# Performance work log

Hardware: AMD Instinct MI355X
Metric: run time of the kernel (lower is better)

## Reference

```python
import jax, jax.numpy as jnp
import numpy as np

ALPHA = 0.34          # Ewald splitting parameter (init kwarg alpha)
MAX_HKL = 12          # init kwarg max_hkl
TWO_PI = 2.0 * np.pi


def setup_inputs() -> dict:
    key = jax.random.key(0)
    k1, k2 = jax.random.split(key)
    N = 4096
    L = 40.0  # cubic box edge (Angstrom)
    coords = jax.random.uniform(k1, (N, 3), dtype=jnp.float32) * L
    q = jax.random.normal(k2, (N,), dtype=jnp.float32)
    q = q - jnp.mean(q)  # neutral cell (k=0 term is excluded)
    box = jnp.eye(3, dtype=jnp.float32) * L
    return {"coords": coords, "box": box, "q": q}


def _ewald_recip_energy(coords, box, q):
    """Reciprocal-space Ewald sum over |h|,|k|,|l| <= MAX_HKL (rank=0 PME fallback).

    pot_i = (4*pi/V) * sum_{k!=0} exp(-|k|^2/(4 a^2))/|k|^2 * Re[S(k) exp(-i k.r_i)]
    E     = 0.5 * sum_i q_i * pot_i
    """
    K = MAX_HKL
    vol = jnp.abs(jnp.linalg.det(box))
    recip = TWO_PI * jnp.linalg.inv(box).T  # rows = reciprocal lattice vectors (3,3)
    h = jnp.arange(-K, K + 1)
    hh, kk, ll = jnp.meshgrid(h, h, h, indexing="ij")
    hkl = jnp.stack([hh.ravel(), kk.ravel(), ll.ravel()], axis=-1).astype(jnp.float32)  # (Nk,3)
    kvecs = hkl @ recip                      # (Nk,3)
    k2 = jnp.sum(kvecs * kvecs, axis=-1)     # (Nk,)
    nonzero = k2 > 0.0                       # mask out k = 0 (static shape, jit-safe)
    k2_safe = jnp.where(nonzero, k2, 1.0)
    inv_4a2 = 1.0 / (4.0 * ALPHA * ALPHA)
    fac = jnp.where(nonzero, jnp.exp(-k2_safe * inv_4a2) / k2_safe, 0.0)  # (Nk,)
    phases = coords @ kvecs.T                # (N, Nk)
    c = jnp.cos(phases)
    s = jnp.sin(phases)
    Sre = q @ c                              # (Nk,) Re S(k)
    Sim = q @ s                              # (Nk,) Im S(k)
    pref = (4.0 * np.pi) / vol
    # Re[S(k) e^{-i k.r_i}] = Sre*cos + Sim*sin
    pot = pref * (c @ (fac * Sre) + s @ (fac * Sim))  # (N,)
    return 0.5 * jnp.sum(q * pot)


def reference(coords, box, q):
    return _ewald_recip_energy(coords, box, q)
```

## Files before the change

### kernel.cpp

```cpp
#include <hip/hip_runtime.h>
#include <math.h>

namespace {
constexpr int   KMAX   = 12;
constexpr int   NLINE  = 313;
constexpr int   NGROUP = NLINE * 5;
constexpr int   NKV    = NGROUP * 5;
constexpr int   NSLICE = 8;
constexpr int   SLICE_CAP = 512;
constexpr int   S2_BLOCKS = (NKV + 255) / 256;
constexpr float ALPHA_  = 0.34f;
constexpr float TWO_PI_ = 6.283185307179586f;
}

__device__ __forceinline__ void cofactors(const float* __restrict__ box,
                                          float C[3][3], float* det) {
  const float b00 = box[0], b01 = box[1], b02 = box[2];
  const float b10 = box[3], b11 = box[4], b12 = box[5];
  const float b20 = box[6], b21 = box[7], b22 = box[8];
  C[0][0] =  (b11 * b22 - b12 * b21);
  C[0][1] = -(b10 * b22 - b12 * b20);
  C[0][2] =  (b10 * b21 - b11 * b20);
  C[1][0] = -(b01 * b22 - b02 * b21);
  C[1][1] =  (b00 * b22 - b02 * b20);
  C[1][2] = -(b00 * b21 - b01 * b20);
  C[2][0] =  (b01 * b12 - b02 * b11);
  C[2][1] = -(b00 * b12 - b02 * b10);
  C[2][2] =  (b00 * b11 - b01 * b10);
  *det = b00 * C[0][0] + b01 * C[0][1] + b02 * C[0][2];
}

__device__ __forceinline__ void line_hk(int L, int* h, int* k) {
  if (L < 300)      { *h = L / 25 + 1; *k = L % 25 - 12; }
  else if (L < 312) { *h = 0;          *k = L - 299;     }
  else              { *h = 0;          *k = 0;           }
}

__global__ __launch_bounds__(256) void ewald_groups(
    const float* __restrict__ coords, const float* __restrict__ box,
    const float* __restrict__ q, int N, float* __restrict__ partial,
    float* __restrict__ out)
{
  __shared__ float4 sf[SLICE_CAP];

  if (blockIdx.x == 0 && blockIdx.y == 0 && threadIdx.x == 0) out[0] = 0.0f;

  float C[3][3], det;
  cofactors(box, C, &det);
  const float invdet = 1.0f / det;

  const int slice = blockIdx.y;
  const int sp    = (N + NSLICE - 1) / NSLICE;
  const int s_beg = slice * sp;
  const int s_end = min(s_beg + sp, N);

  const int lane = threadIdx.x & 63;
  const int g    = blockIdx.x * 4 + (threadIdx.x >> 6);
  const int gc   = (g < NGROUP) ? g : (NGROUP - 1);

  int h, k; line_hk(gc / 5, &h, &k);
  const float hf  = (float)h;
  const float kf  = (float)k;
  const float l0f = (float)(-KMAX + 5 * (gc % 5));

  float Sre[5] = {0.f, 0.f, 0.f, 0.f, 0.f};
  float Sim[5] = {0.f, 0.f, 0.f, 0.f, 0.f};

  for (int cb = s_beg; cb < s_end; cb += SLICE_CAP) {
    const int cnt = min(SLICE_CAP, s_end - cb);
    __syncthreads();
    for (int t = threadIdx.x; t < SLICE_CAP; t += 256) {
      float4 v = make_float4(0.f, 0.f, 0.f, 0.f);
      if (t < cnt) {
        const int gi = cb + t;
        const float x = coords[3 * gi + 0];
        const float y = coords[3 * gi + 1];
        const float z = coords[3 * gi + 2];
        v.x = (x * C[0][0] + y * C[0][1] + z * C[0][2]) * invdet;
        v.y = (x * C[1][0] + y * C[1][1] + z * C[1][2]) * invdet;
        float c = (x * C[2][0] + y * C[2][1] + z * C[2][2]) * invdet;
        v.z = c - floorf(c);
        v.w = q[gi];
      }
      sf[t] = v;
    }
    __syncthreads();

    for (int i = lane; i < SLICE_CAP; i += 64) {
      const float4 p = sf[i];
      float t = fmaf(hf, p.x, fmaf(kf, p.y, l0f * p.z));
      float tf;
      asm("v_fract_f32 %0, %1" : "=v"(tf) : "v"(t));
      float s0, c0, sr, cr;
      asm("v_sin_f32 %0, %1" : "=v"(s0) : "v"(tf));
      asm("v_cos_f32 %0, %1" : "=v"(c0) : "v"(tf));
      asm("v_sin_f32 %0, %1" : "=v"(sr) : "v"(p.z));
      asm("v_cos_f32 %0, %1" : "=v"(cr) : "v"(p.z));
      float Pre = p.w * c0, Pim = p.w * s0;
      Sre[0] += Pre; Sim[0] += Pim;
#pragma unroll
      for (int u = 1; u < 5; ++u) {
        const float nre = fmaf(Pre, cr, -(Pim * sr));
        const float nim = fmaf(Pre, sr,  (Pim * cr));
        Pre = nre; Pim = nim;
        Sre[u] += Pre; Sim[u] += Pim;
      }
    }
  }

#pragma unroll
  for (int off = 32; off > 0; off >>= 1) {
#pragma unroll
    for (int u = 0; u < 5; ++u) {
      Sre[u] += __shfl_down(Sre[u], off);
      Sim[u] += __shfl_down(Sim[u], off);
    }
  }
  if (g < NGROUP && lane == 0) {
    float* dst = partial + (size_t)(g * NSLICE + slice) * 10;
#pragma unroll
    for (int u = 0; u < 5; ++u) {
      dst[2 * u + 0] = Sre[u];
      dst[2 * u + 1] = Sim[u];
    }
  }
}

__global__ __launch_bounds__(256) void stage2(
    const float* __restrict__ partial, const float* __restrict__ box,
    float* __restrict__ out)
{
  __shared__ float red[256];
  const int idx = blockIdx.x * 256 + threadIdx.x;
  float e = 0.f;
  if (idx < NKV) {
    const int g = idx / 5, u = idx % 5;
    const int L = g / 5, sub = g % 5;
    int h, k; line_hk(L, &h, &k);
    const int l = -KMAX + 5 * sub + u;
    if (!(h == 0 && k == 0 && l <= 0)) {
      float re = 0.f, im = 0.f;
      for (int s = 0; s < NSLICE; ++s) {
        const float* p = partial + (size_t)(g * NSLICE + s) * 10 + 2 * u;
        re += p[0]; im += p[1];
      }
      float C[3][3], det;
      cofactors(box, C, &det);
      const float invdet = 1.0f / det;
      const float hf = (float)h, kf = (float)k, lf = (float)l;
      const float kx = (hf * C[0][0] + kf * C[1][0] + lf * C[2][0]) * invdet;
      const float ky = (hf * C[0][1] + kf * C[1][1] + lf * C[2][1]) * invdet;
      const float kz = (hf * C[0][2] + kf * C[1][2] + lf * C[2][2]) * invdet;
      const float k2 = TWO_PI_ * TWO_PI_ * (kx * kx + ky * ky + kz * kz);
      const float fac = __expf(-k2 / (4.0f * ALPHA_ * ALPHA_)) / k2;
      e = fac * fmaf(re, re, im * im);
    }
  }
  red[threadIdx.x] = e;
  __syncthreads();
  for (int s = 128; s > 0; s >>= 1) {
    if (threadIdx.x < s) red[threadIdx.x] += red[threadIdx.x + s];
    __syncthreads();
  }
  if (threadIdx.x == 0) {
    float C[3][3], det;
    cofactors(box, C, &det);
    const float scale = (4.0f * 3.14159265358979323846f) / fabsf(det);
    atomicAdd(out, scale * red[0]);
  }
}

extern "C" void kernel_launch(void* const* d_in, const int* in_sizes, int n_in,
                              void* d_out, int out_size, void* d_ws, size_t ws_size,
                              hipStream_t stream) {
  const float* coords = (const float*)d_in[0];
  const float* box    = (const float*)d_in[1];
  const float* q      = (const float*)d_in[2];
  float* out = (float*)d_out;
  const int N = in_sizes[2];

  float* partial = (float*)d_ws;

  const dim3 grid((NGROUP + 3) / 4, NSLICE);
  hipLaunchKernelGGL(ewald_groups, grid, dim3(256), 0, stream,
                     coords, box, q, N, partial, out);
  hipLaunchKernelGGL(stage2, dim3(S2_BLOCKS), dim3(256), 0, stream,
                     partial, box, out);
}
```

Before: 20.08 us.

## Precompute fractional coordinates in a separate kernel and drop LDS staging

Moves the per-atom conversion to fractional coordinates into a small prepass kernel that writes float4 records to workspace. The main structure-factor kernel then reads them straight from global memory (L2-cached) instead of staging through shared memory with two barriers per chunk, and gets launch bounds that allow higher occupancy. This removes redundant per-block coordinate transforms and syncs, at the cost of an extra kernel launch and a global round trip.

```diff
diff --git a/kernel.cpp b/kernel.cpp
--- a/kernel.cpp
+++ b/kernel.cpp
@@ -7,7 +7,6 @@
 constexpr int   NGROUP = NLINE * 5;
 constexpr int   NKV    = NGROUP * 5;
 constexpr int   NSLICE = 8;
-constexpr int   SLICE_CAP = 512;
 constexpr int   S2_BLOCKS = (NKV + 255) / 256;
 constexpr float ALPHA_  = 0.34f;
 constexpr float TWO_PI_ = 6.283185307179586f;
@@ -36,24 +35,32 @@
   else              { *h = 0;          *k = 0;           }
 }
 
-__global__ __launch_bounds__(256) void ewald_groups(
+__global__ __launch_bounds__(256) void make_frac(
     const float* __restrict__ coords, const float* __restrict__ box,
-    const float* __restrict__ q, int N, float* __restrict__ partial,
+    const float* __restrict__ q, int N, float4* __restrict__ frac,
     float* __restrict__ out)
 {
-  __shared__ float4 sf[SLICE_CAP];
-
-  if (blockIdx.x == 0 && blockIdx.y == 0 && threadIdx.x == 0) out[0] = 0.0f;
-
+  const int i = blockIdx.x * 256 + threadIdx.x;
+  if (i == 0) out[0] = 0.0f;
+  if (i >= N) return;
   float C[3][3], det;
   cofactors(box, C, &det);
   const float invdet = 1.0f / det;
+  const float x = coords[3 * i + 0];
+  const float y = coords[3 * i + 1];
+  const float z = coords[3 * i + 2];
+  float4 f;
+  f.x = (x * C[0][0] + y * C[0][1] + z * C[0][2]) * invdet;
+  f.y = (x * C[1][0] + y * C[1][1] + z * C[1][2]) * invdet;
+  float c = (x * C[2][0] + y * C[2][1] + z * C[2][2]) * invdet;
+  f.z = c - floorf(c);
+  f.w = q[i];
+  frac[i] = f;
+}
 
-  const int slice = blockIdx.y;
-  const int sp    = (N + NSLICE - 1) / NSLICE;
-  const int s_beg = slice * sp;
-  const int s_end = min(s_beg + sp, N);
-
+__global__ __launch_bounds__(256, 8) void ewald_g5(
+    const float4* __restrict__ frac, int N, float* __restrict__ partial)
+{
   const int lane = threadIdx.x & 63;
   const int g    = blockIdx.x * 4 + (threadIdx.x >> 6);
   const int gc   = (g < NGROUP) ? g : (NGROUP - 1);
@@ -63,48 +70,32 @@
   const float kf  = (float)k;
   const float l0f = (float)(-KMAX + 5 * (gc % 5));
 
+  const int slice = blockIdx.y;
+  const int sp    = (N + NSLICE - 1) / NSLICE;
+  const int s_beg = slice * sp;
+  const int s_end = min(s_beg + sp, N);
+
   float Sre[5] = {0.f, 0.f, 0.f, 0.f, 0.f};
   float Sim[5] = {0.f, 0.f, 0.f, 0.f, 0.f};
 
-  for (int cb = s_beg; cb < s_end; cb += SLICE_CAP) {
-    const int cnt = min(SLICE_CAP, s_end - cb);
-    __syncthreads();
-    for (int t = threadIdx.x; t < SLICE_CAP; t += 256) {
-      float4 v = make_float4(0.f, 0.f, 0.f, 0.f);
-      if (t < cnt) {
-        const int gi = cb + t;
-        const float x = coords[3 * gi + 0];
-        const float y = coords[3 * gi + 1];
-        const float z = coords[3 * gi + 2];
-        v.x = (x * C[0][0] + y * C[0][1] + z * C[0][2]) * invdet;
-        v.y = (x * C[1][0] + y * C[1][1] + z * C[1][2]) * invdet;
-        float c = (x * C[2][0] + y * C[2][1] + z * C[2][2]) * invdet;
-        v.z = c - floorf(c);
-        v.w = q[gi];
-      }
-      sf[t] = v;
-    }
-    __syncthreads();
-
-    for (int i = lane; i < SLICE_CAP; i += 64) {
-      const float4 p = sf[i];
-      float t = fmaf(hf, p.x, fmaf(kf, p.y, l0f * p.z));
-      float tf;
-      asm("v_fract_f32 %0, %1" : "=v"(tf) : "v"(t));
-      float s0, c0, sr, cr;
-      asm("v_sin_f32 %0, %1" : "=v"(s0) : "v"(tf));
-      asm("v_cos_f32 %0, %1" : "=v"(c0) : "v"(tf));
-      asm("v_sin_f32 %0, %1" : "=v"(sr) : "v"(p.z));
-      asm("v_cos_f32 %0, %1" : "=v"(cr) : "v"(p.z));
-      float Pre = p.w * c0, Pim = p.w * s0;
-      Sre[0] += Pre; Sim[0] += Pim;
+  for (int i = s_beg + lane; i < s_end; i += 64) {
+    const float4 p = frac[i];
+    float t = fmaf(hf, p.x, fmaf(kf, p.y, l0f * p.z));
+    float tf;
+    asm("v_fract_f32 %0, %1" : "=v"(tf) : "v"(t));
+    float s0, c0, sr, cr;
+    asm("v_sin_f32 %0, %1" : "=v"(s0) : "v"(tf));
+    asm("v_cos_f32 %0, %1" : "=v"(c0) : "v"(tf));
+    asm("v_sin_f32 %0, %1" : "=v"(sr) : "v"(p.z));
+    asm("v_cos_f32 %0, %1" : "=v"(cr) : "v"(p.z));
+    float Pre = p.w * c0, Pim = p.w * s0;
+    Sre[0] += Pre; Sim[0] += Pim;
 #pragma unroll
-      for (int u = 1; u < 5; ++u) {
-        const float nre = fmaf(Pre, cr, -(Pim * sr));
-        const float nim = fmaf(Pre, sr,  (Pim * cr));
-        Pre = nre; Pim = nim;
-        Sre[u] += Pre; Sim[u] += Pim;
-      }
+    for (int u = 1; u < 5; ++u) {
+      const float nre = fmaf(Pre, cr, -(Pim * sr));
+      const float nim = fmaf(Pre, sr,  (Pim * cr));
+      Pre = nre; Pim = nim;
+      Sre[u] += Pre; Sim[u] += Pim;
     }
   }
 
@@ -179,11 +170,13 @@
   float* out = (float*)d_out;
   const int N = in_sizes[2];
 
-  float* partial = (float*)d_ws;
+  float4* frac    = (float4*)d_ws;
+  float*  partial = (float*)((char*)d_ws + (128 << 10));
 
+  hipLaunchKernelGGL(make_frac, dim3((N + 255) / 256), dim3(256), 0, stream,
+                     coords, box, q, N, frac, out);
   const dim3 grid((NGROUP + 3) / 4, NSLICE);
-  hipLaunchKernelGGL(ewald_groups, grid, dim3(256), 0, stream,
-                     coords, box, q, N, partial, out);
+  hipLaunchKernelGGL(ewald_g5, grid, dim3(256), 0, stream, frac, N, partial);
   hipLaunchKernelGGL(stage2, dim3(S2_BLOCKS), dim3(256), 0, stream,
                      partial, box, out);
 }
```

Result: slower. 24.96 us (+24.3%).
